# Kernel optimization log

Measured on AMD Instinct MI355X. Metric: run time of the kernel, lower is better.

Reference implementation:

```python
import jax, jax.numpy as jnp
import numpy as np
from jax import lax

B, T, E, D, CC, K, H = 64, 2000, 512, 1024, 32, 31, 128
PAD = (K - 1) // 2


def setup_inputs() -> dict:
    key = jax.random.key(0)
    ks = jax.random.split(key, 12)
    enc_output = jax.random.normal(ks[0], (B, T, E), dtype=jnp.float32)
    text_len = jax.random.randint(ks[1], (B,), 1, T + 1)
    dec_state = jax.random.normal(ks[2], (B, D), dtype=jnp.float32)
    prev_att_w = jax.random.uniform(ks[3], (B, T), dtype=jnp.float32)
    # learned parameters
    W_enc = jax.random.normal(ks[4], (E, H), dtype=jnp.float32) / np.sqrt(E)
    b_enc = jnp.zeros((H,), dtype=jnp.float32)
    W_dec = jax.random.normal(ks[5], (D, H), dtype=jnp.float32) / np.sqrt(D)
    W_att = jax.random.normal(ks[6], (CC, H), dtype=jnp.float32) / np.sqrt(CC)
    conv_w = jax.random.normal(ks[7], (CC, 1, K), dtype=jnp.float32) / np.sqrt(K)  # OIH
    W_out = jax.random.normal(ks[8], (H, 1), dtype=jnp.float32) / np.sqrt(H)
    b_out = jnp.zeros((1,), dtype=jnp.float32)
    return {
        'enc_output': enc_output, 'text_len': text_len, 'dec_state': dec_state,
        'prev_att_w': prev_att_w, 'W_enc': W_enc, 'b_enc': b_enc, 'W_dec': W_dec,
        'W_att': W_att, 'conv_w': conv_w, 'W_out': W_out, 'b_out': b_out,
    }


def reference(enc_output, text_len, dec_state, prev_att_w,
              W_enc, b_enc, W_dec, W_att, conv_w, W_out, b_out):
    # processed_memory = fc_enc(enc_output): (B,T,H)
    pm = jnp.einsum('bte,eh->bth', enc_output, W_enc) + b_enc
    # location conv: (B,1,T) -> (B,CC,T), same padding, no bias
    att_conv = lax.conv_general_dilated(
        prev_att_w[:, None, :], conv_w, window_strides=(1,),
        padding=[(PAD, PAD)], dimension_numbers=('NCH', 'OIH', 'NCH'))
    # fc_att on channel dim: (B,T,H)
    att_conv = jnp.einsum('bct,ch->bth', att_conv, W_att)
    # fc_dec(dec_state): (B,1,H)
    dec = (dec_state @ W_dec)[:, None, :]
    # energy: (B,T)
    energy = (jnp.tanh(att_conv + pm + dec) @ W_out)[..., 0] + b_out[0]
    att_w = jax.nn.softmax(energy, axis=1)  # (B,T)
    att_c = jnp.einsum('bte,bt->be', enc_output, att_w)  # (B,E)
    return att_c, att_w
```

## Files before the change

### kernel.cpp

```cpp
#include <hip/hip_runtime.h>
#include <hip/hip_fp16.h>

typedef _Float16 f16x8 __attribute__((ext_vector_type(8)));
typedef float f32x4 __attribute__((ext_vector_type(4)));


__device__ __forceinline__ unsigned short f2h(float f) {
  __half h = __float2half(f);
  return __builtin_bit_cast(unsigned short, h);
}

__device__ __forceinline__ f16x8 u4_to_f16x8(uint4 v) {
  return __builtin_bit_cast(f16x8, v);
}

__device__ __forceinline__ f16x8 cvt8(float4 u, float4 v) {
  uint4 w;
  w.x = ((unsigned)f2h(u.y) << 16) | f2h(u.x);
  w.y = ((unsigned)f2h(u.w) << 16) | f2h(u.z);
  w.z = ((unsigned)f2h(v.y) << 16) | f2h(v.x);
  w.w = ((unsigned)f2h(v.w) << 16) | f2h(v.z);
  return u4_to_f16x8(w);
}

__device__ __forceinline__ float fast_tanh(float x) {
  return 1.f - 2.f / (__expf(2.f * x) + 1.f);
}

__global__ __launch_bounds__(256) void prep_kernel(
    const float* __restrict__ dec_state, const float* __restrict__ W_dec,
    const float* __restrict__ b_enc, const float* __restrict__ conv_w,
    const float* __restrict__ W_att, const float* __restrict__ W_enc,
    float* __restrict__ decb, unsigned short* __restrict__ MTg,
    unsigned short* __restrict__ WTpack)
{
  const int blk = blockIdx.x, tid = threadIdx.x;
  if (blk < 32) {
    __shared__ float sd[2048];
    const int sub = tid >> 7, h = tid & 127;
    const int b = blk*2 + sub;
    for (int i = h; i < 1024; i += 128) sd[sub*1024 + i] = dec_state[b*1024 + i];
    __syncthreads();
    float acc = b_enc[h];
    #pragma unroll 8
    for (int d = 0; d < 1024; ++d) acc = fmaf(sd[sub*1024 + d], W_dec[d*128 + h], acc);
    decb[b*128 + h] = acc;
  } else if (blk < 96) {
    const int e0 = (blk - 32) * 8;
    #pragma unroll
    for (int jj = 0; jj < 4; ++jj) {
      int idx = tid + jj*256;
      int el = idx >> 7, hh = idx & 127;
      int e = e0 + el;
      int kc = e >> 6, ks = (e >> 5) & 1, lg = (e >> 3) & 3, j = e & 7;
      int nt = hh >> 4, lr = hh & 15;
      int dst = (((kc*2 + ks)*8 + nt)*64 + lg*16 + lr)*8 + j;
      WTpack[dst] = f2h(W_enc[e*128 + hh]);
    }
  } else {
    if (tid < 128) {
      const int h = tid;
      for (int k = 0; k < 31; ++k) {
        float a = 0.f;
        #pragma unroll
        for (int c = 0; c < 32; ++c) a = fmaf(conv_w[c*31 + k], W_att[c*128 + h], a);
        MTg[h*32 + k] = f2h(a);
      }
      MTg[h*32 + 31] = 0;
    }
  }
}

__global__ __launch_bounds__(1024, 4) void energy_kernel(
    const float* __restrict__ enc, const float* __restrict__ prev,
    const unsigned short* __restrict__ WTpack, const unsigned short* __restrict__ MTg,
    const float* __restrict__ decb, const float* __restrict__ W_out,
    float* __restrict__ energy)
{
  extern __shared__ __align__(16) char smem[];
  unsigned short* sWT = (unsigned short*)smem;
  unsigned short* sMT = (unsigned short*)(smem + 131072);
  float* sPrev = (float*)(smem + 139264);
  float* sDecb = (float*)(smem + 140416);
  float* sWout = (float*)(smem + 140928);

  const int b  = blockIdx.y;
  const int t0 = blockIdx.x * 256;
  const int tid = threadIdx.x;
  const int wave = tid >> 6, lane = tid & 63;
  const int lr = lane & 15, lg = lane >> 4;

  {
    const uint4* wsrc = (const uint4*)WTpack;
    uint4* wdst = (uint4*)sWT;
    #pragma unroll
    for (int i = 0; i < 8; ++i) wdst[tid + i*1024] = wsrc[tid + i*1024];
    if (tid < 512) ((uint4*)sMT)[tid] = ((const uint4*)MTg)[tid];
    if (tid < 288) {
      int tt = t0 + tid - 15;
      sPrev[tid] = (tt >= 0 && tt < 2000) ? prev[b*2000 + tt] : 0.f;
    }
    if (tid < 128) { sDecb[tid] = decb[b*128 + tid]; sWout[tid] = W_out[tid]; }
  }
  __syncthreads();

  const float* encB = enc + (size_t)b * (2000u*512u);
  int tg = t0 + wave*16 + lr; if (tg > 1999) tg = 1999;
  const float* rowp = encB + (size_t)tg*512 + lg*8;
  const char* wlds = (const char*)sWT + lane*16;

  f32x4 acc[8];
  #pragma unroll
  for (int i = 0; i < 8; ++i) acc[i] = (f32x4){0,0,0,0};

  float4 c0 = *reinterpret_cast<const float4*>(rowp + 0);
  float4 c1 = *reinterpret_cast<const float4*>(rowp + 4);
  float4 c2 = *reinterpret_cast<const float4*>(rowp + 32);
  float4 c3 = *reinterpret_cast<const float4*>(rowp + 36);

  #pragma unroll
  for (int kc = 0; kc < 8; ++kc) {
    float4 n0, n1, n2, n3;
    if (kc < 7) {
      const float* p = rowp + (kc+1)*64;
      n0 = *reinterpret_cast<const float4*>(p + 0);
      n1 = *reinterpret_cast<const float4*>(p + 4);
      n2 = *reinterpret_cast<const float4*>(p + 32);
      n3 = *reinterpret_cast<const float4*>(p + 36);
    }
    f16x8 a0 = cvt8(c0, c1);
    f16x8 a1 = cvt8(c2, c3);
    #pragma unroll
    for (int nt = 0; nt < 8; ++nt) {
      uint4 rb = *reinterpret_cast<const uint4*>(wlds + ((kc*2 + 0)*8 + nt)*1024);
      acc[nt] = __builtin_amdgcn_mfma_f32_16x16x32_f16(a0, u4_to_f16x8(rb), acc[nt], 0, 0, 0);
    }
    #pragma unroll
    for (int nt = 0; nt < 8; ++nt) {
      uint4 rb = *reinterpret_cast<const uint4*>(wlds + ((kc*2 + 1)*8 + nt)*1024);
      acc[nt] = __builtin_amdgcn_mfma_f32_16x16x32_f16(a1, u4_to_f16x8(rb), acc[nt], 0, 0, 0);
    }
    if (kc < 7) { c0 = n0; c1 = n1; c2 = n2; c3 = n3; }
  }

  {
    f16x8 a2;
    const int pb0 = wave*16 + lr + lg*8;
    #pragma unroll
    for (int j = 0; j < 8; ++j)
      a2[j] = __builtin_bit_cast(_Float16, f2h(sPrev[pb0 + j]));
    const char* mlds = (const char*)sMT + lr*64 + lg*16;
    #pragma unroll
    for (int nt = 0; nt < 8; ++nt) {
      uint4 mv = *reinterpret_cast<const uint4*>(mlds + nt*1024);
      acc[nt] = __builtin_amdgcn_mfma_f32_16x16x32_f16(a2, u4_to_f16x8(mv), acc[nt], 0, 0, 0);
    }
  }

  {
    float es0 = 0.f, es1 = 0.f, es2 = 0.f, es3 = 0.f;
    #pragma unroll
    for (int nt = 0; nt < 8; ++nt) {
      float dh = sDecb[nt*16 + lr];
      float wo = sWout[nt*16 + lr];
      es0 += fast_tanh(acc[nt][0] + dh) * wo;
      es1 += fast_tanh(acc[nt][1] + dh) * wo;
      es2 += fast_tanh(acc[nt][2] + dh) * wo;
      es3 += fast_tanh(acc[nt][3] + dh) * wo;
    }
    #pragma unroll
    for (int off = 1; off < 16; off <<= 1) {
      es0 += __shfl_xor(es0, off, 64);
      es1 += __shfl_xor(es1, off, 64);
      es2 += __shfl_xor(es2, off, 64);
      es3 += __shfl_xor(es3, off, 64);
    }
    if (lr == 0) {
      const int t = t0 + wave*16 + lg*4;
      float ev[4] = {es0, es1, es2, es3};
      #pragma unroll
      for (int r = 0; r < 4; ++r)
        if (t + r < 2000) energy[b*2000 + t + r] = ev[r];
    }
  }
}

__global__ __launch_bounds__(256) void softmax_kernel(
    const float* __restrict__ energy, float* __restrict__ attw)
{
  const int b = blockIdx.x, tid = threadIdx.x;
  __shared__ float red[4];
  __shared__ float red2[4];
  float m = -1e30f;
  for (int i = tid; i < 2000; i += 256) m = fmaxf(m, energy[b*2000 + i]);
  #pragma unroll
  for (int off = 1; off < 64; off <<= 1) m = fmaxf(m, __shfl_xor(m, off, 64));
  if ((tid & 63) == 0) red[tid >> 6] = m;
  __syncthreads();
  m = fmaxf(fmaxf(red[0], red[1]), fmaxf(red[2], red[3]));

  float s = 0.f;
  for (int i = tid; i < 2000; i += 256) {
    float p = __expf(energy[b*2000 + i] - m);
    attw[b*2000 + i] = p;
    s += p;
  }
  #pragma unroll
  for (int off = 1; off < 64; off <<= 1) s += __shfl_xor(s, off, 64);
  if ((tid & 63) == 0) red2[tid >> 6] = s;
  __syncthreads();
  s = red2[0] + red2[1] + red2[2] + red2[3];
  float inv = 1.f / s;
  for (int i = tid; i < 2000; i += 256) attw[b*2000 + i] *= inv;
}

__global__ __launch_bounds__(256) void attc_partial_kernel(
    const float* __restrict__ enc, const float* __restrict__ attw,
    float* __restrict__ part)
{
  const int b = blockIdx.y, ch = blockIdx.x, tid = threadIdx.x;
  const int p = tid >> 7;
  const int e4 = (tid & 127) * 4;
  const int tstart = ch * 125 + p, tend = ch * 125 + 125;
  const float* encB = enc + (size_t)b * (2000u*512u);
  float a0 = 0.f, a1 = 0.f, a2 = 0.f, a3 = 0.f;
  #pragma unroll 2
  for (int t = tstart; t < tend; t += 2) {
    float w = attw[b*2000 + t];
    float4 v = *reinterpret_cast<const float4*>(encB + (size_t)t*512 + e4);
    a0 = fmaf(v.x, w, a0);
    a1 = fmaf(v.y, w, a1);
    a2 = fmaf(v.z, w, a2);
    a3 = fmaf(v.w, w, a3);
  }
  float4 out = {a0, a1, a2, a3};
  *reinterpret_cast<float4*>(part + ((size_t)(b*32 + ch*2 + p))*512 + e4) = out;
}

__global__ __launch_bounds__(128) void attc_reduce_kernel(
    const float* __restrict__ part, float* __restrict__ out)
{
  const int b = blockIdx.x, e4 = threadIdx.x * 4;
  float4 s = {0.f, 0.f, 0.f, 0.f};
  #pragma unroll
  for (int c = 0; c < 32; ++c) {
    float4 v = *reinterpret_cast<const float4*>(part + ((size_t)(b*32 + c))*512 + e4);
    s.x += v.x; s.y += v.y; s.z += v.z; s.w += v.w;
  }
  *reinterpret_cast<float4*>(out + b*512 + e4) = s;
}

extern "C" void kernel_launch(void* const* d_in, const int* in_sizes, int n_in,
                              void* d_out, int out_size, void* d_ws, size_t ws_size,
                              hipStream_t stream) {
  (void)in_sizes; (void)n_in; (void)out_size; (void)ws_size;
  const float* enc       = (const float*)d_in[0];
  const float* dec_state = (const float*)d_in[2];
  const float* prev      = (const float*)d_in[3];
  const float* W_enc     = (const float*)d_in[4];
  const float* b_enc     = (const float*)d_in[5];
  const float* W_dec     = (const float*)d_in[6];
  const float* W_att     = (const float*)d_in[7];
  const float* conv_w    = (const float*)d_in[8];
  const float* W_out     = (const float*)d_in[9];

  char* ws = (char*)d_ws;
  float*          energy = (float*)(ws + 0);
  float*          decb   = (float*)(ws + 524288);
  unsigned short* MTg    = (unsigned short*)(ws + 557056);
  unsigned short* WTpack = (unsigned short*)(ws + 565248);
  float*          part   = (float*)(ws + 696320);

  float* attc = (float*)d_out;
  float* attw = (float*)d_out + 64*512;

  const int lds_bytes = 141440;

  prep_kernel        <<<97, 256, 0, stream>>>(dec_state, W_dec, b_enc, conv_w, W_att, W_enc,
                                              decb, MTg, WTpack);
  energy_kernel      <<<dim3(8, 64), 1024, lds_bytes, stream>>>(enc, prev, WTpack, MTg, decb, W_out, energy);
  softmax_kernel     <<<64, 256, 0, stream>>>(energy, attw);
  attc_partial_kernel<<<dim3(16, 64), 256, 0, stream>>>(enc, attw, part);
  attc_reduce_kernel <<<64, 128, 0, stream>>>(part, attc);
}
```

Before: 156.5 us.

## Pre-pack encoder output to fp16 MFMA layout before energy kernel

Adds a pack kernel that converts enc_output to fp16 and writes it in the MFMA A-operand fragment layout in workspace. A new energy kernel then reads contiguous 16-byte fragments with software prefetch instead of converting fp32 on the fly. This adds a full extra pass over the encoder tensor (read fp32, write fp16) and a large workspace requirement, and falls back to the old path if the workspace is too small.

```diff
diff --git a/kernel.cpp b/kernel.cpp
--- a/kernel.cpp
+++ b/kernel.cpp
@@ -67,6 +67,142 @@
         MTg[h*32 + k] = f2h(a);
       }
       MTg[h*32 + 31] = 0;
+    }
+  }
+}
+
+__global__ __launch_bounds__(256) void pack_kernel(
+    const float* __restrict__ enc, unsigned short* __restrict__ PK)
+{
+  const int b  = blockIdx.y;
+  const int t0c = blockIdx.x * 256;
+  const int tid = threadIdx.x;
+  const int e4 = (tid & 127) * 4;
+  const int kc = e4 >> 6, ks = (e4 >> 5) & 1, lg = (e4 >> 3) & 3, jh = e4 & 7;
+  const float* encB = enc + (size_t)b * (2000u*512u);
+  char* pkB = (char*)PK + (size_t)(b*8 + blockIdx.x)*16*16384;
+  #pragma unroll 4
+  for (int c = 0; c < 32; ++c) {
+    int row = 2*c + (tid >> 7);
+    #pragma unroll
+    for (int q = 0; q < 4; ++q) {
+      int lrow = q*64 + row;
+      int t = t0c + lrow;
+      int src = t > 1999 ? 1999 : t;
+      float4 v = *reinterpret_cast<const float4*>(encB + (size_t)src*512 + e4);
+      uint2 wv;
+      wv.x = ((unsigned)f2h(v.y) << 16) | f2h(v.x);
+      wv.y = ((unsigned)f2h(v.w) << 16) | f2h(v.z);
+      int w = lrow >> 4, lr = lrow & 15;
+      char* dst = pkB + (size_t)w*16384 + kc*2048 + ks*1024 + (lg*16 + lr)*16 + jh*2;
+      *reinterpret_cast<uint2*>(dst) = wv;
+    }
+  }
+}
+
+__global__ __launch_bounds__(1024, 4) void energy_pk_kernel(
+    const unsigned short* __restrict__ PK, const float* __restrict__ prev,
+    const unsigned short* __restrict__ WTpack, const unsigned short* __restrict__ MTg,
+    const float* __restrict__ decb, const float* __restrict__ W_out,
+    float* __restrict__ energy)
+{
+  extern __shared__ __align__(16) char smem[];
+  unsigned short* sWT = (unsigned short*)smem;
+  unsigned short* sMT = (unsigned short*)(smem + 131072);
+  float* sPrev = (float*)(smem + 139264);
+  float* sDecb = (float*)(smem + 140416);
+  float* sWout = (float*)(smem + 140928);
+
+  const int b  = blockIdx.y;
+  const int t0 = blockIdx.x * 256;
+  const int tid = threadIdx.x;
+  const int wave = tid >> 6, lane = tid & 63;
+  const int lr = lane & 15, lg = lane >> 4;
+
+  {
+    const uint4* wsrc = (const uint4*)WTpack;
+    uint4* wdst = (uint4*)sWT;
+    #pragma unroll
+    for (int i = 0; i < 8; ++i) wdst[tid + i*1024] = wsrc[tid + i*1024];
+    if (tid < 512) ((uint4*)sMT)[tid] = ((const uint4*)MTg)[tid];
+    if (tid < 288) {
+      int tt = t0 + tid - 15;
+      sPrev[tid] = (tt >= 0 && tt < 2000) ? prev[b*2000 + tt] : 0.f;
+    }
+    if (tid < 128) { sDecb[tid] = decb[b*128 + tid]; sWout[tid] = W_out[tid]; }
+  }
+  __syncthreads();
+
+  const char* apk = (const char*)PK + (size_t)((b*8 + blockIdx.x)*16 + wave)*16384 + lane*16;
+  const char* wlds = (const char*)sWT + lane*16;
+
+  f32x4 acc[8];
+  #pragma unroll
+  for (int i = 0; i < 8; ++i) acc[i] = (f32x4){0,0,0,0};
+
+  uint4 c0 = *reinterpret_cast<const uint4*>(apk + 0);
+  uint4 c1 = *reinterpret_cast<const uint4*>(apk + 1024);
+
+  #pragma unroll
+  for (int kc = 0; kc < 8; ++kc) {
+    uint4 n0, n1;
+    if (kc < 7) {
+      n0 = *reinterpret_cast<const uint4*>(apk + (kc+1)*2048);
+      n1 = *reinterpret_cast<const uint4*>(apk + (kc+1)*2048 + 1024);
+    }
+    f16x8 a0 = u4_to_f16x8(c0);
+    f16x8 a1 = u4_to_f16x8(c1);
+    #pragma unroll
+    for (int nt = 0; nt < 8; ++nt) {
+      uint4 rb = *reinterpret_cast<const uint4*>(wlds + ((kc*2 + 0)*8 + nt)*1024);
+      acc[nt] = __builtin_amdgcn_mfma_f32_16x16x32_f16(a0, u4_to_f16x8(rb), acc[nt], 0, 0, 0);
+    }
+    #pragma unroll
+    for (int nt = 0; nt < 8; ++nt) {
+      uint4 rb = *reinterpret_cast<const uint4*>(wlds + ((kc*2 + 1)*8 + nt)*1024);
+      acc[nt] = __builtin_amdgcn_mfma_f32_16x16x32_f16(a1, u4_to_f16x8(rb), acc[nt], 0, 0, 0);
+    }
+    if (kc < 7) { c0 = n0; c1 = n1; }
+  }
+
+  {
+    f16x8 a2;
+    const int pb0 = wave*16 + lr + lg*8;
+    #pragma unroll
+    for (int j = 0; j < 8; ++j)
+      a2[j] = __builtin_bit_cast(_Float16, f2h(sPrev[pb0 + j]));
+    const char* mlds = (const char*)sMT + lr*64 + lg*16;
+    #pragma unroll
+    for (int nt = 0; nt < 8; ++nt) {
+      uint4 mv = *reinterpret_cast<const uint4*>(mlds + nt*1024);
+      acc[nt] = __builtin_amdgcn_mfma_f32_16x16x32_f16(a2, u4_to_f16x8(mv), acc[nt], 0, 0, 0);
+    }
+  }
+
+  {
+    float es0 = 0.f, es1 = 0.f, es2 = 0.f, es3 = 0.f;
+    #pragma unroll
+    for (int nt = 0; nt < 8; ++nt) {
+      float dh = sDecb[nt*16 + lr];
+      float wo = sWout[nt*16 + lr];
+      es0 += fast_tanh(acc[nt][0] + dh) * wo;
+      es1 += fast_tanh(acc[nt][1] + dh) * wo;
+      es2 += fast_tanh(acc[nt][2] + dh) * wo;
+      es3 += fast_tanh(acc[nt][3] + dh) * wo;
+    }
+    #pragma unroll
+    for (int off = 1; off < 16; off <<= 1) {
+      es0 += __shfl_xor(es0, off, 64);
+      es1 += __shfl_xor(es1, off, 64);
+      es2 += __shfl_xor(es2, off, 64);
+      es3 += __shfl_xor(es3, off, 64);
+    }
+    if (lr == 0) {
+      const int t = t0 + wave*16 + lg*4;
+      float ev[4] = {es0, es1, es2, es3};
+      #pragma unroll
+      for (int r = 0; r < 4; ++r)
+        if (t + r < 2000) energy[b*2000 + t + r] = ev[r];
     }
   }
 }
@@ -253,7 +389,7 @@
 extern "C" void kernel_launch(void* const* d_in, const int* in_sizes, int n_in,
                               void* d_out, int out_size, void* d_ws, size_t ws_size,
                               hipStream_t stream) {
-  (void)in_sizes; (void)n_in; (void)out_size; (void)ws_size;
+  (void)in_sizes; (void)n_in; (void)out_size;
   const float* enc       = (const float*)d_in[0];
   const float* dec_state = (const float*)d_in[2];
   const float* prev      = (const float*)d_in[3];
@@ -270,15 +406,23 @@
   unsigned short* MTg    = (unsigned short*)(ws + 557056);
   unsigned short* WTpack = (unsigned short*)(ws + 565248);
   float*          part   = (float*)(ws + 696320);
+  unsigned short* PK     = (unsigned short*)(ws + 4890624);
+
+  const size_t need_pk = 4890624ull + 134217728ull;
 
   float* attc = (float*)d_out;
   float* attw = (float*)d_out + 64*512;
 
   const int lds_bytes = 141440;
 
-  prep_kernel        <<<97, 256, 0, stream>>>(dec_state, W_dec, b_enc, conv_w, W_att, W_enc,
-                                              decb, MTg, WTpack);
-  energy_kernel      <<<dim3(8, 64), 1024, lds_bytes, stream>>>(enc, prev, WTpack, MTg, decb, W_out, energy);
+  prep_kernel<<<97, 256, 0, stream>>>(dec_state, W_dec, b_enc, conv_w, W_att, W_enc,
+                                      decb, MTg, WTpack);
+  if (ws_size >= need_pk) {
+    pack_kernel     <<<dim3(8, 64), 256, 0, stream>>>(enc, PK);
+    energy_pk_kernel<<<dim3(8, 64), 1024, lds_bytes, stream>>>(PK, prev, WTpack, MTg, decb, W_out, energy);
+  } else {
+    energy_kernel   <<<dim3(8, 64), 1024, lds_bytes, stream>>>(enc, prev, WTpack, MTg, decb, W_out, energy);
+  }
   softmax_kernel     <<<64, 256, 0, stream>>>(energy, attw);
   attc_partial_kernel<<<dim3(16, 64), 256, 0, stream>>>(enc, attw, part);
   attc_reduce_kernel <<<64, 128, 0, stream>>>(part, attc);
```

Measured after the change: 269.0 us. +71.9%, slower.

## Stage encoder rows through swizzled LDS with coalesced loads and split-K weight staging

Applied to the files above, without the earlier changes.

The energy kernel moves from 1024-thread blocks covering 256 timesteps to 512-thread blocks covering 128 timesteps. Each wave now loads whole encoder rows with coalesced float4 reads, converts them to fp16, and writes them into an XOR-swizzled LDS tile, replacing per-lane strided global reads. The K dimension is split into two halves so only half of W_enc is held in LDS at a time, and the second half of both activations and weights is prefetched into registers while the first half's MFMAs run. The aim is better global memory coalescing and overlap of loads with compute. In exchange the grid doubles, so every block re-reads the weight matrix, and large LDS use still limits each CU to one block of fewer waves.

```diff
diff --git a/kernel.cpp b/kernel.cpp
--- a/kernel.cpp
+++ b/kernel.cpp
@@ -12,15 +12,6 @@
 
 __device__ __forceinline__ f16x8 u4_to_f16x8(uint4 v) {
   return __builtin_bit_cast(f16x8, v);
-}
-
-__device__ __forceinline__ f16x8 cvt8(float4 u, float4 v) {
-  uint4 w;
-  w.x = ((unsigned)f2h(u.y) << 16) | f2h(u.x);
-  w.y = ((unsigned)f2h(u.w) << 16) | f2h(u.z);
-  w.z = ((unsigned)f2h(v.y) << 16) | f2h(v.x);
-  w.w = ((unsigned)f2h(v.w) << 16) | f2h(v.z);
-  return u4_to_f16x8(w);
 }
 
 __device__ __forceinline__ float fast_tanh(float x) {
@@ -71,76 +62,128 @@
   }
 }
 
-__global__ __launch_bounds__(1024, 4) void energy_kernel(
+__global__ __launch_bounds__(512, 2) void energy_kernel(
     const float* __restrict__ enc, const float* __restrict__ prev,
     const unsigned short* __restrict__ WTpack, const unsigned short* __restrict__ MTg,
     const float* __restrict__ decb, const float* __restrict__ W_out,
     float* __restrict__ energy)
 {
   extern __shared__ __align__(16) char smem[];
-  unsigned short* sWT = (unsigned short*)smem;
+  char* sB = smem;
+  char* sA = smem + 65536;
   unsigned short* sMT = (unsigned short*)(smem + 131072);
   float* sPrev = (float*)(smem + 139264);
-  float* sDecb = (float*)(smem + 140416);
-  float* sWout = (float*)(smem + 140928);
+  float* sDecb = (float*)(smem + 139904);
+  float* sWout = (float*)(smem + 140416);
 
   const int b  = blockIdx.y;
-  const int t0 = blockIdx.x * 256;
+  const int t0 = blockIdx.x * 128;
   const int tid = threadIdx.x;
   const int wave = tid >> 6, lane = tid & 63;
   const int lr = lane & 15, lg = lane >> 4;
 
+  const float* encB = enc + (size_t)b * (2000u*512u);
+
+  uint4 rb[8];
   {
     const uint4* wsrc = (const uint4*)WTpack;
-    uint4* wdst = (uint4*)sWT;
-    #pragma unroll
-    for (int i = 0; i < 8; ++i) wdst[tid + i*1024] = wsrc[tid + i*1024];
-    if (tid < 512) ((uint4*)sMT)[tid] = ((const uint4*)MTg)[tid];
-    if (tid < 288) {
-      int tt = t0 + tid - 15;
-      sPrev[tid] = (tt >= 0 && tt < 2000) ? prev[b*2000 + tt] : 0.f;
-    }
-    if (tid < 128) { sDecb[tid] = decb[b*128 + tid]; sWout[tid] = W_out[tid]; }
-  }
-  __syncthreads();
-
-  const float* encB = enc + (size_t)b * (2000u*512u);
-  int tg = t0 + wave*16 + lr; if (tg > 1999) tg = 1999;
-  const float* rowp = encB + (size_t)tg*512 + lg*8;
-  const char* wlds = (const char*)sWT + lane*16;
+    #pragma unroll
+    for (int i = 0; i < 8; ++i) rb[i] = wsrc[tid + i*512];
+  }
+  float4 ra[16];
+  #pragma unroll
+  for (int i = 0; i < 16; ++i) {
+    int row = t0 + wave*16 + i; if (row > 1999) row = 1999;
+    ra[i] = *reinterpret_cast<const float4*>(encB + (size_t)row*512 + lane*4);
+  }
+  ((uint4*)sMT)[tid] = ((const uint4*)MTg)[tid & 511];
+  if (tid < 160) {
+    int tt = t0 + tid - 15;
+    sPrev[tid] = (tt >= 0 && tt < 2000) ? prev[b*2000 + tt] : 0.f;
+  }
+  if (tid < 128) { sDecb[tid] = decb[b*128 + tid]; sWout[tid] = W_out[tid]; }
+  {
+    uint4* wdst = (uint4*)sB;
+    #pragma unroll
+    for (int i = 0; i < 8; ++i) wdst[tid + i*512] = rb[i];
+  }
+  char* aw = sA + wave*8192;
+  #pragma unroll
+  for (int i = 0; i < 16; ++i) {
+    uint2 wv;
+    wv.x = ((unsigned)f2h(ra[i].y) << 16) | f2h(ra[i].x);
+    wv.y = ((unsigned)f2h(ra[i].w) << 16) | f2h(ra[i].z);
+    *reinterpret_cast<uint2*>(aw + i*512 + ((lane*8) ^ ((i & 7) << 4))) = wv;
+  }
+  __syncthreads();
 
   f32x4 acc[8];
   #pragma unroll
   for (int i = 0; i < 8; ++i) acc[i] = (f32x4){0,0,0,0};
 
-  float4 c0 = *reinterpret_cast<const float4*>(rowp + 0);
-  float4 c1 = *reinterpret_cast<const float4*>(rowp + 4);
-  float4 c2 = *reinterpret_cast<const float4*>(rowp + 32);
-  float4 c3 = *reinterpret_cast<const float4*>(rowp + 36);
-
-  #pragma unroll
-  for (int kc = 0; kc < 8; ++kc) {
-    float4 n0, n1, n2, n3;
-    if (kc < 7) {
-      const float* p = rowp + (kc+1)*64;
-      n0 = *reinterpret_cast<const float4*>(p + 0);
-      n1 = *reinterpret_cast<const float4*>(p + 4);
-      n2 = *reinterpret_cast<const float4*>(p + 32);
-      n3 = *reinterpret_cast<const float4*>(p + 36);
-    }
-    f16x8 a0 = cvt8(c0, c1);
-    f16x8 a1 = cvt8(c2, c3);
-    #pragma unroll
-    for (int nt = 0; nt < 8; ++nt) {
-      uint4 rb = *reinterpret_cast<const uint4*>(wlds + ((kc*2 + 0)*8 + nt)*1024);
-      acc[nt] = __builtin_amdgcn_mfma_f32_16x16x32_f16(a0, u4_to_f16x8(rb), acc[nt], 0, 0, 0);
-    }
-    #pragma unroll
-    for (int nt = 0; nt < 8; ++nt) {
-      uint4 rb = *reinterpret_cast<const uint4*>(wlds + ((kc*2 + 1)*8 + nt)*1024);
-      acc[nt] = __builtin_amdgcn_mfma_f32_16x16x32_f16(a1, u4_to_f16x8(rb), acc[nt], 0, 0, 0);
-    }
-    if (kc < 7) { c0 = n0; c1 = n1; c2 = n2; c3 = n3; }
+  const char* ar = sA + wave*8192 + lr*512;
+  const int sw = (lr & 7) << 4;
+
+  float4 na[16];
+  #pragma unroll
+  for (int i = 0; i < 16; ++i) {
+    int row = t0 + wave*16 + i; if (row > 1999) row = 1999;
+    na[i] = *reinterpret_cast<const float4*>(encB + (size_t)row*512 + 256 + lane*4);
+  }
+  uint4 nb[8];
+  {
+    const uint4* wsrc = (const uint4*)WTpack + 4096;
+    #pragma unroll
+    for (int i = 0; i < 8; ++i) nb[i] = wsrc[tid + i*512];
+  }
+
+  #pragma unroll
+  for (int kc = 0; kc < 4; ++kc) {
+    f16x8 a0 = *reinterpret_cast<const f16x8*>(ar + ((kc*128 + 0  + lg*16) ^ sw));
+    f16x8 a1 = *reinterpret_cast<const f16x8*>(ar + ((kc*128 + 64 + lg*16) ^ sw));
+    #pragma unroll
+    for (int nt = 0; nt < 8; ++nt) {
+      uint4 rv = *reinterpret_cast<const uint4*>(sB + ((kc*2 + 0)*8 + nt)*1024 + lane*16);
+      acc[nt] = __builtin_amdgcn_mfma_f32_16x16x32_f16(a0, u4_to_f16x8(rv), acc[nt], 0, 0, 0);
+    }
+    #pragma unroll
+    for (int nt = 0; nt < 8; ++nt) {
+      uint4 rv = *reinterpret_cast<const uint4*>(sB + ((kc*2 + 1)*8 + nt)*1024 + lane*16);
+      acc[nt] = __builtin_amdgcn_mfma_f32_16x16x32_f16(a1, u4_to_f16x8(rv), acc[nt], 0, 0, 0);
+    }
+  }
+
+  asm volatile("s_waitcnt lgkmcnt(0)" ::: "memory");
+  __builtin_amdgcn_sched_barrier(0);
+  #pragma unroll
+  for (int i = 0; i < 16; ++i) {
+    uint2 wv;
+    wv.x = ((unsigned)f2h(na[i].y) << 16) | f2h(na[i].x);
+    wv.y = ((unsigned)f2h(na[i].w) << 16) | f2h(na[i].z);
+    *reinterpret_cast<uint2*>(aw + i*512 + ((lane*8) ^ ((i & 7) << 4))) = wv;
+  }
+  __syncthreads();
+  {
+    uint4* wdst = (uint4*)sB;
+    #pragma unroll
+    for (int i = 0; i < 8; ++i) wdst[tid + i*512] = nb[i];
+  }
+  __syncthreads();
+
+  #pragma unroll
+  for (int kcl = 0; kcl < 4; ++kcl) {
+    f16x8 a0 = *reinterpret_cast<const f16x8*>(ar + ((kcl*128 + 0  + lg*16) ^ sw));
+    f16x8 a1 = *reinterpret_cast<const f16x8*>(ar + ((kcl*128 + 64 + lg*16) ^ sw));
+    #pragma unroll
+    for (int nt = 0; nt < 8; ++nt) {
+      uint4 rv = *reinterpret_cast<const uint4*>(sB + ((kcl*2 + 0)*8 + nt)*1024 + lane*16);
+      acc[nt] = __builtin_amdgcn_mfma_f32_16x16x32_f16(a0, u4_to_f16x8(rv), acc[nt], 0, 0, 0);
+    }
+    #pragma unroll
+    for (int nt = 0; nt < 8; ++nt) {
+      uint4 rv = *reinterpret_cast<const uint4*>(sB + ((kcl*2 + 1)*8 + nt)*1024 + lane*16);
+      acc[nt] = __builtin_amdgcn_mfma_f32_16x16x32_f16(a1, u4_to_f16x8(rv), acc[nt], 0, 0, 0);
+    }
   }
 
   {
@@ -274,11 +317,11 @@
   float* attc = (float*)d_out;
   float* attw = (float*)d_out + 64*512;
 
-  const int lds_bytes = 141440;
+  const int lds_bytes = 140928;
 
   prep_kernel        <<<97, 256, 0, stream>>>(dec_state, W_dec, b_enc, conv_w, W_att, W_enc,
                                               decb, MTg, WTpack);
-  energy_kernel      <<<dim3(8, 64), 1024, lds_bytes, stream>>>(enc, prev, WTpack, MTg, decb, W_out, energy);
+  energy_kernel      <<<dim3(16, 64), 512, lds_bytes, stream>>>(enc, prev, WTpack, MTg, decb, W_out, energy);
   softmax_kernel     <<<64, 256, 0, stream>>>(energy, attw);
   attc_partial_kernel<<<dim3(16, 64), 256, 0, stream>>>(enc, attw, part);
   attc_reduce_kernel <<<64, 128, 0, stream>>>(part, attc);
```

Result: slower. 217.5 us (+39.0%).
